# Kernel tuning notes

Hardware: AMD Instinct MI355X
Metric: run time of the kernel (lower is better)

The kernel has to match this reference:

```python
import jax, jax.numpy as jnp
import numpy as np

N_E = 1024      # nconcepts (codebook size)
E_DIM = 64      # cdim (codebook vector dim)
BETA = 0.25
LEGACY = True


def setup_inputs() -> dict:
    key = jax.random.key(0)
    k1, k2, k3 = jax.random.split(key, 3)
    z_ = jax.random.normal(k1, (32, 256, 32, 32), jnp.float32)
    # 1x1 conv dis_modulator: 256 -> 64 channels (stored as [out, in])
    conv_w = jax.random.normal(k2, (64, 256), jnp.float32) / np.sqrt(256.0)
    conv_b = jnp.zeros((64,), jnp.float32)
    # embedding.weight.data.uniform_(-1/n_e, 1/n_e)
    emb = jax.random.uniform(k3, (N_E, E_DIM), jnp.float32, -1.0 / N_E, 1.0 / N_E)
    return {"z_": z_, "conv_w": conv_w, "conv_b": conv_b, "emb": emb}


def _forward(z_, conv_w, conv_b, emb):
    sg = jax.lax.stop_gradient
    # dis_modulator: 1x1 conv == per-pixel linear map  (B,Cin,H,W)->(B,Cout,H,W)
    z = jnp.einsum('bchw,oc->bohw', z_, conv_w) + conv_b[None, :, None, None]
    B = z.shape[0]
    # torch .view(-1, e_dim): row-major flatten of (B,C,H,W) into chunks of e_dim
    zf = z.reshape(-1, E_DIM)  # [B*C*H*W/e_dim, e_dim]

    # contrastive term: mean pairwise cosine similarity of codebook rows
    d1 = emb @ emb.T                                  # [n_e, n_e]
    norms = jnp.linalg.norm(emb, axis=1)              # [n_e]
    cosine = d1 / (norms[:, None] * norms[None, :])
    contrastive = jnp.mean(cosine)

    # squared L2 distances: ||z||^2 + ||e||^2 - 2 z.e
    d = (jnp.sum(zf * zf, axis=1, keepdims=True)
         + jnp.sum(emb * emb, axis=1)[None, :]
         - 2.0 * (zf @ emb.T))                        # [N, n_e]
    idx = jnp.argmin(d, axis=1)                       # [N]
    z_q = emb[idx].reshape(z.shape)

    if LEGACY:
        loss = jnp.mean((sg(z_q) - z) ** 2) + BETA * jnp.mean((z_q - sg(z)) ** 2)
    else:
        loss = BETA * jnp.mean((sg(z_q) - z) ** 2) + jnp.mean((z_q - sg(z)) ** 2)
    # hessian_penalty(G, z_, G_z=z): G is an affine 1x1 conv, so the central
    # second difference G(z+x) - 2G(z) + G(z-x) is identically zero -> penalty = 0.
    loss = loss + contrastive

    # straight-through estimator
    z_q_st = z + sg(z_q - z)

    # replicate source exactly: flat zeros(B*n_e) scattered at codebook indices
    sampled = jnp.zeros((B * N_E,), z.dtype).at[idx].set(1.0).reshape(B, N_E)
    min_idx = idx.reshape(B, -1)
    return z_q_st, loss, sampled, min_idx


def reference(z_, conv_w, conv_b, emb):
    z_q, loss, sampled, min_idx = _forward(z_, conv_w, conv_b, emb)
    return z_q, loss, sampled, min_idx
```

## Files before the change

kernel.cpp:

```cpp
#include <hip/hip_runtime.h>
#include <hip/hip_bf16.h>

#define BATCH   32
#define CIN     256
#define COUT    64
#define HW      1024
#define NE      1024
#define ED      64
#define NROW    32768
#define ZTOT    2097152

#define OFF_LOSS 2097152
#define OFF_SAMP 2097153
#define OFF_IDX  2129921

#define XSTR 68
#define ESTR 132

__global__ __launch_bounds__(256) void k_init(float* __restrict__ out_samp,
                                              const float* __restrict__ emb,
                                              float* __restrict__ enorm,
                                              float* __restrict__ invn) {
    int b = blockIdx.x;
    if (b < 128) {
        int i = b * 256 + threadIdx.x;
        out_samp[i] = 0.0f;
    } else {
        int j = (b - 128) * 256 + threadIdx.x;
        const float* e = emb + j * ED;
        float r8[8];
        #pragma unroll
        for (int s = 0; s < 8; s++) { float x = e[s]; r8[s] = x * x; }
        #pragma unroll
        for (int m = 1; m < 8; m++) {
            #pragma unroll
            for (int s = 0; s < 8; s++) { float x = e[8 * m + s]; r8[s] += x * x; }
        }
        float en = ((r8[0] + r8[1]) + (r8[2] + r8[3])) + ((r8[4] + r8[5]) + (r8[6] + r8[7]));
        enorm[j] = en;
        invn[j]  = 1.0f / sqrtf(en);
    }
}

__global__ __launch_bounds__(256) void k_contrast(const float* __restrict__ emb,
                                                  const float* __restrict__ invn,
                                                  float* __restrict__ cpart) {
    int t = threadIdx.x;
    int b = blockIdx.x;
    int d = t & 63, q = t >> 6;
    int i0 = b * 64;
    float s = 0.0f;
    #pragma unroll
    for (int m = 0; m < 16; m++) {
        int i = i0 + q + 4 * m;
        s = fmaf(emb[i * ED + d], invn[i], s);
    }
    __shared__ float S[256];
    S[t] = s;
    __syncthreads();
    if (t < 64)
        cpart[b * 64 + t] = (S[t] + S[t + 64]) + (S[t + 128] + S[t + 192]);
}

__global__ __launch_bounds__(256) void k_conv(const float* __restrict__ x,
                                              const float* __restrict__ w,
                                              const float* __restrict__ bias,
                                              float* __restrict__ z) {
    __shared__ float Xs[64 * XSTR];
    __shared__ float Ws[64 * XSTR];
    int t  = threadIdx.x;
    int b  = blockIdx.y;
    int p0 = blockIdx.x * 64;
    int pg = t & 15;
    int og = t >> 4;
    float acc[4][4];
    #pragma unroll
    for (int i = 0; i < 4; i++)
        #pragma unroll
        for (int j = 0; j < 4; j++) acc[i][j] = 0.0f;

    for (int c0 = 0; c0 < CIN; c0 += 64) {
        __syncthreads();
        {
            int u = t & 15, cg2 = t >> 4;
            #pragma unroll
            for (int m = 0; m < 4; m++) {
                int c = cg2 + 16 * m;
                float4 v = *(const float4*)&x[(size_t)(b * CIN + c0 + c) * HW + p0 + 4 * u];
                *(float4*)&Xs[c * XSTR + 4 * u] = v;
            }
            #pragma unroll
            for (int m = 0; m < 4; m++) {
                int o = cg2 + 16 * m;
                float4 v = *(const float4*)&w[o * CIN + c0 + 4 * u];
                Ws[(4 * u + 0) * XSTR + o] = v.x;
                Ws[(4 * u + 1) * XSTR + o] = v.y;
                Ws[(4 * u + 2) * XSTR + o] = v.z;
                Ws[(4 * u + 3) * XSTR + o] = v.w;
            }
        }
        __syncthreads();
        #pragma unroll 8
        for (int k = 0; k < 64; k++) {
            float4 xv = *(const float4*)&Xs[k * XSTR + 4 * pg];
            float4 wv = *(const float4*)&Ws[k * XSTR + 4 * og];
            float xa[4] = {xv.x, xv.y, xv.z, xv.w};
            float wb[4] = {wv.x, wv.y, wv.z, wv.w};
            #pragma unroll
            for (int i = 0; i < 4; i++)
                #pragma unroll
                for (int j = 0; j < 4; j++)
                    acc[i][j] = fmaf(xa[i], wb[j], acc[i][j]);
        }
    }
    #pragma unroll
    for (int j = 0; j < 4; j++) {
        int o = 4 * og + j;
        float bv = bias[o];
        float4 out;
        out.x = acc[0][j] + bv;
        out.y = acc[1][j] + bv;
        out.z = acc[2][j] + bv;
        out.w = acc[3][j] + bv;
        *(float4*)&z[(size_t)(b * COUT + o) * HW + p0 + 4 * pg] = out;
    }
}

__global__ __launch_bounds__(256) void k_dist(const float* __restrict__ z,
                                              const float* __restrict__ emb,
                                              const float* __restrict__ enorm,
                                              float* __restrict__ out_idx,
                                              float* __restrict__ out_samp,
                                              float* __restrict__ out_zq,
                                              float* __restrict__ ssep) {
    __shared__ float zs[64 * XSTR];
    __shared__ float es[64 * ESTR];
    __shared__ float zn_s[64];
    __shared__ float en_s[128];
    __shared__ float redd_s[16 * 64];
    __shared__ int   redj_s[16 * 64];
    __shared__ int   bj_s[64];
    __shared__ float warr[4];
    int t = threadIdx.x;
    int row0 = blockIdx.x * 64;
    int rg = t & 15;
    int cg = t >> 4;

    {
        int k = t & 63, wv = t >> 6;
        #pragma unroll
        for (int m = 0; m < 4; m++) {
            int v = wv + 4 * m;
            float4 val;
            val.x = z[(size_t)(row0 + 4 * v + 0) * ED + k];
            val.y = z[(size_t)(row0 + 4 * v + 1) * ED + k];
            val.z = z[(size_t)(row0 + 4 * v + 2) * ED + k];
            val.w = z[(size_t)(row0 + 4 * v + 3) * ED + k];
            *(float4*)&zs[k * XSTR + 4 * v] = val;
        }
    }
    if (t < 64) {
        const float* zr = z + (size_t)(row0 + t) * ED;
        float r8[8];
        #pragma unroll
        for (int s = 0; s < 8; s++) { float xx = zr[s]; r8[s] = xx * xx; }
        #pragma unroll
        for (int m = 1; m < 8; m++) {
            #pragma unroll
            for (int s = 0; s < 8; s++) { float xx = zr[8 * m + s]; r8[s] += xx * xx; }
        }
        zn_s[t] = ((r8[0] + r8[1]) + (r8[2] + r8[3])) + ((r8[4] + r8[5]) + (r8[6] + r8[7]));
    }

    float bestd[4];
    int   bestj[4];
    #pragma unroll
    for (int i = 0; i < 4; i++) { bestd[i] = __builtin_huge_valf(); bestj[i] = 0; }

    for (int ch = 0; ch < 8; ch++) {
        int c0 = ch * 128;
        __syncthreads();
        {
            int k = t & 63, wv = t >> 6;
            #pragma unroll
            for (int m = 0; m < 8; m++) {
                int v = wv + 4 * m;
                float4 val;
                val.x = emb[(size_t)(c0 + 4 * v + 0) * ED + k];
                val.y = emb[(size_t)(c0 + 4 * v + 1) * ED + k];
                val.z = emb[(size_t)(c0 + 4 * v + 2) * ED + k];
                val.w = emb[(size_t)(c0 + 4 * v + 3) * ED + k];
                *(float4*)&es[k * ESTR + 4 * v] = val;
            }
            if (t < 32) {
                float4 ev4 = *(const float4*)&enorm[c0 + 4 * t];
                *(float4*)&en_s[4 * t] = ev4;
            }
        }
        __syncthreads();

        float acc[4][8];
        #pragma unroll
        for (int i = 0; i < 4; i++)
            #pragma unroll
            for (int j = 0; j < 8; j++) acc[i][j] = 0.0f;

        #pragma unroll 8
        for (int k = 0; k < 64; k++) {
            float4 xv = *(const float4*)&zs[k * XSTR + 4 * rg];
            float4 e0 = *(const float4*)&es[k * ESTR + 8 * cg];
            float4 e1 = *(const float4*)&es[k * ESTR + 8 * cg + 4];
            float xa[4] = {xv.x, xv.y, xv.z, xv.w};
            float eb[8] = {e0.x, e0.y, e0.z, e0.w, e1.x, e1.y, e1.z, e1.w};
            #pragma unroll
            for (int i = 0; i < 4; i++)
                #pragma unroll
                for (int j = 0; j < 8; j++)
                    acc[i][j] = fmaf(xa[i], eb[j], acc[i][j]);
        }

        #pragma unroll
        for (int i = 0; i < 4; i++) {
            float zn = zn_s[4 * rg + i];
            #pragma unroll
            for (int j = 0; j < 8; j++) {
                int cl = 8 * cg + j;
                float A = zn + en_s[cl];
                float D = A - 2.0f * acc[i][j];
                if (D < bestd[i]) { bestd[i] = D; bestj[i] = c0 + cl; }
            }
        }
    }

    #pragma unroll
    for (int i = 0; i < 4; i++) {
        redd_s[cg * 64 + 4 * rg + i] = bestd[i];
        redj_s[cg * 64 + 4 * rg + i] = bestj[i];
    }
    __syncthreads();
    if (t < 64) {
        float bd = __builtin_huge_valf();
        int   bj = 0x7fffffff;
        #pragma unroll
        for (int c = 0; c < 16; c++) {
            float dd = redd_s[c * 64 + t];
            int   jj = redj_s[c * 64 + t];
            if (dd < bd || (dd == bd && jj < bj)) { bd = dd; bj = jj; }
        }
        int rowg = row0 + t;
        bj_s[t]       = bj;
        out_idx[rowg] = (float)bj;
        atomicExch(&out_samp[bj], 1.0f);
    }
    __syncthreads();

    {
        int r  = t & 63;
        int kq = t >> 6;
        int bj = bj_s[r];
        const float* er = emb + (size_t)bj * ED + kq * 16;
        float sq = 0.0f;
        #pragma unroll
        for (int m = 0; m < 4; m++) {
            float4 ev = *(const float4*)&er[4 * m];
            float zv0 = zs[(kq * 16 + 4 * m + 0) * XSTR + r];
            float zv1 = zs[(kq * 16 + 4 * m + 1) * XSTR + r];
            float zv2 = zs[(kq * 16 + 4 * m + 2) * XSTR + r];
            float zv3 = zs[(kq * 16 + 4 * m + 3) * XSTR + r];
            float d0 = ev.x - zv0, d1 = ev.y - zv1, d2 = ev.z - zv2, d3 = ev.w - zv3;
            float4 o4;
            o4.x = zv0 + d0; o4.y = zv1 + d1; o4.z = zv2 + d2; o4.w = zv3 + d3;
            *(float4*)&out_zq[(size_t)(row0 + r) * ED + kq * 16 + 4 * m] = o4;
            sq += d0 * d0; sq += d1 * d1; sq += d2 * d2; sq += d3 * d3;
        }
        #pragma unroll
        for (int off = 32; off > 0; off >>= 1) sq += __shfl_down(sq, off, 64);
        int lane = t & 63, wv = t >> 6;
        if (lane == 0) warr[wv] = sq;
    }
    __syncthreads();
    if (t == 0)
        ssep[blockIdx.x] = (warr[0] + warr[1]) + (warr[2] + warr[3]);
}

__global__ __launch_bounds__(256) void k_final(const float* __restrict__ ssep,
                                               const float* __restrict__ cpart,
                                               float* __restrict__ out_loss) {
    __shared__ double SD[256];
    __shared__ float  CS;
    int t = threadIdx.x;
    SD[t] = (double)ssep[t] + (double)ssep[t + 256];
    __syncthreads();
    #pragma unroll
    for (int off = 128; off > 0; off >>= 1) {
        if (t < off) SD[t] += SD[t + off];
        __syncthreads();
    }
    if (t < 64) {
        float v = 0.0f;
        #pragma unroll
        for (int m = 0; m < 16; m++) v += cpart[m * 64 + t];
        float sq = v * v;
        #pragma unroll
        for (int off = 32; off > 0; off >>= 1) sq += __shfl_down(sq, off, 64);
        if (t == 0) CS = sq / (1024.0f * 1024.0f);
    }
    __syncthreads();
    if (t == 0) {
        float m = (float)(SD[0] / (double)ZTOT);
        float loss = m + 0.25f * m;
        out_loss[0] = loss + CS;
    }
}

extern "C" void kernel_launch(void* const* d_in, const int* in_sizes, int n_in,
                              void* d_out, int out_size, void* d_ws, size_t ws_size,
                              hipStream_t stream) {
    (void)in_sizes; (void)n_in; (void)out_size; (void)ws_size;
    const float* z_     = (const float*)d_in[0];
    const float* conv_w = (const float*)d_in[1];
    const float* conv_b = (const float*)d_in[2];
    const float* emb    = (const float*)d_in[3];

    float* out      = (float*)d_out;
    float* out_zq   = out;
    float* out_loss = out + OFF_LOSS;
    float* out_samp = out + OFF_SAMP;
    float* out_idx  = out + OFF_IDX;

    char*  ws       = (char*)d_ws;
    float* wz       = (float*)ws;
    float* enorm    = (float*)(ws + 8388608);
    float* invn     = enorm + 1024;
    float* cpart    = (float*)(ws + 8396800);
    float* ssep     = (float*)(ws + 8400896);

    k_init    <<<132, 256, 0, stream>>>(out_samp, emb, enorm, invn);
    k_contrast<<<16,  256, 0, stream>>>(emb, invn, cpart);
    k_conv    <<<dim3(16, 32), 256, 0, stream>>>(z_, conv_w, conv_b, wz);
    k_dist    <<<512, 256, 0, stream>>>(wz, emb, enorm, out_idx, out_samp, out_zq, ssep);
    k_final   <<<1, 256, 0, stream>>>(ssep, cpart, out_loss);
}
```

Baseline: 166.3 us.

## Merge init/contrast/conv into one launch and enlarge conv and distance tiles

Folds the sampled-buffer zeroing, codebook norms, contrastive partial sums and the 1x1 conv into a single k_pre launch that branches on block index, dropping two kernel launches. Conv tiles grow to 128 pixels per block (8x4 per thread) and the distance kernel handles 128 rows by 256 codes per chunk with an 8x16 per-thread accumulator, which raises register reuse but leaves only 256 blocks at one block per CU. The z-norm now reads from shared memory, and the reduction buffers reuse the codebook tile storage. The larger accumulators may push up register pressure and lower occupancy.

```diff
diff --git a/kernel.cpp b/kernel.cpp
--- a/kernel.cpp
+++ b/kernel.cpp
@@ -1,5 +1,4 @@
 #include <hip/hip_runtime.h>
-#include <hip/hip_bf16.h>
 
 #define BATCH   32
 #define CIN     256
@@ -14,100 +13,118 @@
 #define OFF_SAMP 2097153
 #define OFF_IDX  2129921
 
-#define XSTR 68
-#define ESTR 132
-
-__global__ __launch_bounds__(256) void k_init(float* __restrict__ out_samp,
-                                              const float* __restrict__ emb,
-                                              float* __restrict__ enorm,
-                                              float* __restrict__ invn) {
-    int b = blockIdx.x;
-    if (b < 128) {
-        int i = b * 256 + threadIdx.x;
-        out_samp[i] = 0.0f;
-    } else {
-        int j = (b - 128) * 256 + threadIdx.x;
-        const float* e = emb + j * ED;
+#define CXSTR 132
+#define CWSTR 68
+#define ZSTR  132
+#define ESTR2 260
+
+__global__ __launch_bounds__(256, 2) void k_pre(const float* __restrict__ x,
+                                                const float* __restrict__ w,
+                                                const float* __restrict__ bias,
+                                                float* __restrict__ z,
+                                                const float* __restrict__ emb,
+                                                float* __restrict__ out_samp,
+                                                float* __restrict__ enorm,
+                                                float* __restrict__ cpart) {
+    __shared__ float SH[64 * CXSTR + 64 * CWSTR];
+    int bx = blockIdx.x;
+    int t  = threadIdx.x;
+
+    if (bx < 128) {
+        out_samp[bx * 256 + t] = 0.0f;
+        return;
+    }
+    if (bx < 144) {
+        float* invl = SH;
+        float* S    = SH + 64;
+        int b2 = bx - 128;
+        int i0 = b2 * 64;
+        if (t < 64) {
+            const float* e = emb + (size_t)(i0 + t) * ED;
+            float r8[8];
+            #pragma unroll
+            for (int s = 0; s < 8; s++) { float xx = e[s]; r8[s] = xx * xx; }
+            #pragma unroll
+            for (int m = 1; m < 8; m++) {
+                #pragma unroll
+                for (int s = 0; s < 8; s++) { float xx = e[8 * m + s]; r8[s] += xx * xx; }
+            }
+            float en = ((r8[0] + r8[1]) + (r8[2] + r8[3])) + ((r8[4] + r8[5]) + (r8[6] + r8[7]));
+            invl[t] = 1.0f / sqrtf(en);
+        }
+        __syncthreads();
+        int d = t & 63, q = t >> 6;
+        float s = 0.0f;
+        #pragma unroll
+        for (int m = 0; m < 16; m++) {
+            int il = q + 4 * m;
+            s = fmaf(emb[(size_t)(i0 + il) * ED + d], invl[il], s);
+        }
+        S[t] = s;
+        __syncthreads();
+        if (t < 64)
+            cpart[b2 * 64 + t] = (S[t] + S[t + 64]) + (S[t + 128] + S[t + 192]);
+        return;
+    }
+    if (bx < 148) {
+        int j = (bx - 144) * 256 + t;
+        const float* e = emb + (size_t)j * ED;
         float r8[8];
         #pragma unroll
-        for (int s = 0; s < 8; s++) { float x = e[s]; r8[s] = x * x; }
+        for (int s = 0; s < 8; s++) { float xx = e[s]; r8[s] = xx * xx; }
         #pragma unroll
         for (int m = 1; m < 8; m++) {
             #pragma unroll
-            for (int s = 0; s < 8; s++) { float x = e[8 * m + s]; r8[s] += x * x; }
-        }
-        float en = ((r8[0] + r8[1]) + (r8[2] + r8[3])) + ((r8[4] + r8[5]) + (r8[6] + r8[7]));
-        enorm[j] = en;
-        invn[j]  = 1.0f / sqrtf(en);
-    }
-}
-
-__global__ __launch_bounds__(256) void k_contrast(const float* __restrict__ emb,
-                                                  const float* __restrict__ invn,
-                                                  float* __restrict__ cpart) {
-    int t = threadIdx.x;
-    int b = blockIdx.x;
-    int d = t & 63, q = t >> 6;
-    int i0 = b * 64;
-    float s = 0.0f;
-    #pragma unroll
-    for (int m = 0; m < 16; m++) {
-        int i = i0 + q + 4 * m;
-        s = fmaf(emb[i * ED + d], invn[i], s);
-    }
-    __shared__ float S[256];
-    S[t] = s;
-    __syncthreads();
-    if (t < 64)
-        cpart[b * 64 + t] = (S[t] + S[t + 64]) + (S[t + 128] + S[t + 192]);
-}
-
-__global__ __launch_bounds__(256) void k_conv(const float* __restrict__ x,
-                                              const float* __restrict__ w,
-                                              const float* __restrict__ bias,
-                                              float* __restrict__ z) {
-    __shared__ float Xs[64 * XSTR];
-    __shared__ float Ws[64 * XSTR];
-    int t  = threadIdx.x;
-    int b  = blockIdx.y;
-    int p0 = blockIdx.x * 64;
-    int pg = t & 15;
-    int og = t >> 4;
-    float acc[4][4];
-    #pragma unroll
-    for (int i = 0; i < 4; i++)
+            for (int s = 0; s < 8; s++) { float xx = e[8 * m + s]; r8[s] += xx * xx; }
+        }
+        enorm[j] = ((r8[0] + r8[1]) + (r8[2] + r8[3])) + ((r8[4] + r8[5]) + (r8[6] + r8[7]));
+        return;
+    }
+
+    float* Xs = SH;
+    float* Ws = SH + 64 * CXSTR;
+    int cbx = bx - 148;
+    int b   = cbx >> 3;
+    int p0  = (cbx & 7) * 128;
+    int pg  = t & 15;
+    int og  = t >> 4;
+    float acc[8][4];
+    #pragma unroll
+    for (int i = 0; i < 8; i++)
         #pragma unroll
         for (int j = 0; j < 4; j++) acc[i][j] = 0.0f;
 
     for (int c0 = 0; c0 < CIN; c0 += 64) {
         __syncthreads();
         {
-            int u = t & 15, cg2 = t >> 4;
+            int u = t & 31, cc = t >> 5;
+            #pragma unroll
+            for (int m = 0; m < 8; m++) {
+                int c = cc + 8 * m;
+                float4 v = *(const float4*)&x[(size_t)(b * CIN + c0 + c) * HW + p0 + 4 * u];
+                *(float4*)&Xs[c * CXSTR + 4 * u] = v;
+            }
+            int u2 = t & 15, o2 = t >> 4;
             #pragma unroll
             for (int m = 0; m < 4; m++) {
-                int c = cg2 + 16 * m;
-                float4 v = *(const float4*)&x[(size_t)(b * CIN + c0 + c) * HW + p0 + 4 * u];
-                *(float4*)&Xs[c * XSTR + 4 * u] = v;
-            }
-            #pragma unroll
-            for (int m = 0; m < 4; m++) {
-                int o = cg2 + 16 * m;
-                float4 v = *(const float4*)&w[o * CIN + c0 + 4 * u];
-                Ws[(4 * u + 0) * XSTR + o] = v.x;
-                Ws[(4 * u + 1) * XSTR + o] = v.y;
-                Ws[(4 * u + 2) * XSTR + o] = v.z;
-                Ws[(4 * u + 3) * XSTR + o] = v.w;
-            }
-        }
-        __syncthreads();
-        #pragma unroll 8
+                int o = o2 + 16 * m;
+                float4 v = *(const float4*)&w[o * CIN + c0 + 4 * u2];
+                Ws[(4 * u2 + 0) * CWSTR + o] = v.x;
+                Ws[(4 * u2 + 1) * CWSTR + o] = v.y;
+                Ws[(4 * u2 + 2) * CWSTR + o] = v.z;
+                Ws[(4 * u2 + 3) * CWSTR + o] = v.w;
+            }
+        }
+        __syncthreads();
+        #pragma unroll 4
         for (int k = 0; k < 64; k++) {
-            float4 xv = *(const float4*)&Xs[k * XSTR + 4 * pg];
-            float4 wv = *(const float4*)&Ws[k * XSTR + 4 * og];
-            float xa[4] = {xv.x, xv.y, xv.z, xv.w};
-            float wb[4] = {wv.x, wv.y, wv.z, wv.w};
-            #pragma unroll
-            for (int i = 0; i < 4; i++)
+            float4 xa4 = *(const float4*)&Xs[k * CXSTR + 4 * pg];
+            float4 xb4 = *(const float4*)&Xs[k * CXSTR + 64 + 4 * pg];
+            float4 wv4 = *(const float4*)&Ws[k * CWSTR + 4 * og];
+            float xa[8] = {xa4.x, xa4.y, xa4.z, xa4.w, xb4.x, xb4.y, xb4.z, xb4.w};
+            float wb[4] = {wv4.x, wv4.y, wv4.z, wv4.w};
+            #pragma unroll
+            for (int i = 0; i < 8; i++)
                 #pragma unroll
                 for (int j = 0; j < 4; j++)
                     acc[i][j] = fmaf(xa[i], wb[j], acc[i][j]);
@@ -117,114 +134,120 @@
     for (int j = 0; j < 4; j++) {
         int o = 4 * og + j;
         float bv = bias[o];
-        float4 out;
-        out.x = acc[0][j] + bv;
-        out.y = acc[1][j] + bv;
-        out.z = acc[2][j] + bv;
-        out.w = acc[3][j] + bv;
-        *(float4*)&z[(size_t)(b * COUT + o) * HW + p0 + 4 * pg] = out;
+        float4 lo, hi;
+        lo.x = acc[0][j] + bv; lo.y = acc[1][j] + bv;
+        lo.z = acc[2][j] + bv; lo.w = acc[3][j] + bv;
+        hi.x = acc[4][j] + bv; hi.y = acc[5][j] + bv;
+        hi.z = acc[6][j] + bv; hi.w = acc[7][j] + bv;
+        *(float4*)&z[(size_t)(b * COUT + o) * HW + p0 + 4 * pg]      = lo;
+        *(float4*)&z[(size_t)(b * COUT + o) * HW + p0 + 64 + 4 * pg] = hi;
     }
 }
 
-__global__ __launch_bounds__(256) void k_dist(const float* __restrict__ z,
-                                              const float* __restrict__ emb,
-                                              const float* __restrict__ enorm,
-                                              float* __restrict__ out_idx,
-                                              float* __restrict__ out_samp,
-                                              float* __restrict__ out_zq,
-                                              float* __restrict__ ssep) {
-    __shared__ float zs[64 * XSTR];
-    __shared__ float es[64 * ESTR];
-    __shared__ float zn_s[64];
-    __shared__ float en_s[128];
-    __shared__ float redd_s[16 * 64];
-    __shared__ int   redj_s[16 * 64];
-    __shared__ int   bj_s[64];
+__global__ __launch_bounds__(256, 1) void k_dist(const float* __restrict__ z,
+                                                 const float* __restrict__ emb,
+                                                 const float* __restrict__ enorm,
+                                                 float* __restrict__ out_idx,
+                                                 float* __restrict__ out_samp,
+                                                 float* __restrict__ out_zq,
+                                                 float* __restrict__ ssep) {
+    __shared__ float zs[64 * ZSTR];
+    __shared__ float es[64 * ESTR2];
+    __shared__ float zn_s[128];
+    __shared__ float en_s[256];
     __shared__ float warr[4];
+    float* redd_s = es;
+    int*   redj_s = (int*)(es + 2048);
+    int*   bj_s   = (int*)(es + 4096);
     int t = threadIdx.x;
-    int row0 = blockIdx.x * 64;
+    int row0 = blockIdx.x * 128;
     int rg = t & 15;
     int cg = t >> 4;
 
     {
         int k = t & 63, wv = t >> 6;
         #pragma unroll
-        for (int m = 0; m < 4; m++) {
+        for (int m = 0; m < 8; m++) {
             int v = wv + 4 * m;
             float4 val;
             val.x = z[(size_t)(row0 + 4 * v + 0) * ED + k];
             val.y = z[(size_t)(row0 + 4 * v + 1) * ED + k];
             val.z = z[(size_t)(row0 + 4 * v + 2) * ED + k];
             val.w = z[(size_t)(row0 + 4 * v + 3) * ED + k];
-            *(float4*)&zs[k * XSTR + 4 * v] = val;
-        }
-    }
-    if (t < 64) {
-        const float* zr = z + (size_t)(row0 + t) * ED;
+            *(float4*)&zs[k * ZSTR + 4 * v] = val;
+        }
+    }
+    __syncthreads();
+    if (t < 128) {
         float r8[8];
         #pragma unroll
-        for (int s = 0; s < 8; s++) { float xx = zr[s]; r8[s] = xx * xx; }
+        for (int s = 0; s < 8; s++) { float xx = zs[s * ZSTR + t]; r8[s] = xx * xx; }
         #pragma unroll
         for (int m = 1; m < 8; m++) {
             #pragma unroll
-            for (int s = 0; s < 8; s++) { float xx = zr[8 * m + s]; r8[s] += xx * xx; }
+            for (int s = 0; s < 8; s++) { float xx = zs[(8 * m + s) * ZSTR + t]; r8[s] += xx * xx; }
         }
         zn_s[t] = ((r8[0] + r8[1]) + (r8[2] + r8[3])) + ((r8[4] + r8[5]) + (r8[6] + r8[7]));
     }
 
-    float bestd[4];
-    int   bestj[4];
-    #pragma unroll
-    for (int i = 0; i < 4; i++) { bestd[i] = __builtin_huge_valf(); bestj[i] = 0; }
-
-    for (int ch = 0; ch < 8; ch++) {
-        int c0 = ch * 128;
+    float bestd[8];
+    int   bestj[8];
+    #pragma unroll
+    for (int i = 0; i < 8; i++) { bestd[i] = __builtin_huge_valf(); bestj[i] = 0; }
+
+    for (int ch = 0; ch < 4; ch++) {
+        int c0 = ch * 256;
         __syncthreads();
         {
             int k = t & 63, wv = t >> 6;
             #pragma unroll
-            for (int m = 0; m < 8; m++) {
+            for (int m = 0; m < 16; m++) {
                 int v = wv + 4 * m;
                 float4 val;
                 val.x = emb[(size_t)(c0 + 4 * v + 0) * ED + k];
                 val.y = emb[(size_t)(c0 + 4 * v + 1) * ED + k];
                 val.z = emb[(size_t)(c0 + 4 * v + 2) * ED + k];
                 val.w = emb[(size_t)(c0 + 4 * v + 3) * ED + k];
-                *(float4*)&es[k * ESTR + 4 * v] = val;
-            }
-            if (t < 32) {
+                *(float4*)&es[k * ESTR2 + 4 * v] = val;
+            }
+            if (t < 64) {
                 float4 ev4 = *(const float4*)&enorm[c0 + 4 * t];
                 *(float4*)&en_s[4 * t] = ev4;
             }
         }
         __syncthreads();
 
-        float acc[4][8];
-        #pragma unroll
-        for (int i = 0; i < 4; i++)
-            #pragma unroll
-            for (int j = 0; j < 8; j++) acc[i][j] = 0.0f;
-
-        #pragma unroll 8
+        float acc[8][16];
+        #pragma unroll
+        for (int i = 0; i < 8; i++)
+            #pragma unroll
+            for (int j = 0; j < 16; j++) acc[i][j] = 0.0f;
+
+        #pragma unroll 2
         for (int k = 0; k < 64; k++) {
-            float4 xv = *(const float4*)&zs[k * XSTR + 4 * rg];
-            float4 e0 = *(const float4*)&es[k * ESTR + 8 * cg];
-            float4 e1 = *(const float4*)&es[k * ESTR + 8 * cg + 4];
-            float xa[4] = {xv.x, xv.y, xv.z, xv.w};
-            float eb[8] = {e0.x, e0.y, e0.z, e0.w, e1.x, e1.y, e1.z, e1.w};
-            #pragma unroll
-            for (int i = 0; i < 4; i++)
+            float4 za = *(const float4*)&zs[k * ZSTR + 4 * rg];
+            float4 zb = *(const float4*)&zs[k * ZSTR + 64 + 4 * rg];
+            float4 e0 = *(const float4*)&es[k * ESTR2 + 16 * cg];
+            float4 e1 = *(const float4*)&es[k * ESTR2 + 16 * cg + 4];
+            float4 e2 = *(const float4*)&es[k * ESTR2 + 16 * cg + 8];
+            float4 e3 = *(const float4*)&es[k * ESTR2 + 16 * cg + 12];
+            float xa[8]  = {za.x, za.y, za.z, za.w, zb.x, zb.y, zb.z, zb.w};
+            float eb[16] = {e0.x, e0.y, e0.z, e0.w, e1.x, e1.y, e1.z, e1.w,
+                            e2.x, e2.y, e2.z, e2.w, e3.x, e3.y, e3.z, e3.w};
+            #pragma unroll
+            for (int i = 0; i < 8; i++)
                 #pragma unroll
-                for (int j = 0; j < 8; j++)
+                for (int j = 0; j < 16; j++)
                     acc[i][j] = fmaf(xa[i], eb[j], acc[i][j]);
         }
 
         #pragma unroll
-        for (int i = 0; i < 4; i++) {
-            float zn = zn_s[4 * rg + i];
-            #pragma unroll
-            for (int j = 0; j < 8; j++) {
-                int cl = 8 * cg + j;
+        for (int i = 0; i < 8; i++) {
+            int rl = (i < 4) ? (4 * rg + i) : (64 + 4 * rg + (i - 4));
+            float zn = zn_s[rl];
+            #pragma unroll
+            for (int j = 0; j < 16; j++) {
+                int cl = 16 * cg + j;
                 float A = zn + en_s[cl];
                 float D = A - 2.0f * acc[i][j];
                 if (D < bestd[i]) { bestd[i] = D; bestj[i] = c0 + cl; }
@@ -232,19 +255,21 @@
         }
     }
 
-    #pragma unroll
-    for (int i = 0; i < 4; i++) {
-        redd_s[cg * 64 + 4 * rg + i] = bestd[i];
-        redj_s[cg * 64 + 4 * rg + i] = bestj[i];
-    }
-    __syncthreads();
-    if (t < 64) {
+    __syncthreads();
+    #pragma unroll
+    for (int i = 0; i < 8; i++) {
+        int rl = (i < 4) ? (4 * rg + i) : (64 + 4 * rg + (i - 4));
+        redd_s[cg * 128 + rl] = bestd[i];
+        redj_s[cg * 128 + rl] = bestj[i];
+    }
+    __syncthreads();
+    if (t < 128) {
         float bd = __builtin_huge_valf();
         int   bj = 0x7fffffff;
         #pragma unroll
         for (int c = 0; c < 16; c++) {
-            float dd = redd_s[c * 64 + t];
-            int   jj = redj_s[c * 64 + t];
+            float dd = redd_s[c * 128 + t];
+            int   jj = redj_s[c * 128 + t];
             if (dd < bd || (dd == bd && jj < bj)) { bd = dd; bj = jj; }
         }
         int rowg = row0 + t;
@@ -255,28 +280,28 @@
     __syncthreads();
 
     {
-        int r  = t & 63;
-        int kq = t >> 6;
+        int r  = t & 127;
+        int kq = t >> 7;
         int bj = bj_s[r];
-        const float* er = emb + (size_t)bj * ED + kq * 16;
+        const float* er = emb + (size_t)bj * ED + kq * 32;
         float sq = 0.0f;
         #pragma unroll
-        for (int m = 0; m < 4; m++) {
+        for (int m = 0; m < 8; m++) {
             float4 ev = *(const float4*)&er[4 * m];
-            float zv0 = zs[(kq * 16 + 4 * m + 0) * XSTR + r];
-            float zv1 = zs[(kq * 16 + 4 * m + 1) * XSTR + r];
-            float zv2 = zs[(kq * 16 + 4 * m + 2) * XSTR + r];
-            float zv3 = zs[(kq * 16 + 4 * m + 3) * XSTR + r];
+            int kk = kq * 32 + 4 * m;
+            float zv0 = zs[(kk + 0) * ZSTR + r];
+            float zv1 = zs[(kk + 1) * ZSTR + r];
+            float zv2 = zs[(kk + 2) * ZSTR + r];
+            float zv3 = zs[(kk + 3) * ZSTR + r];
             float d0 = ev.x - zv0, d1 = ev.y - zv1, d2 = ev.z - zv2, d3 = ev.w - zv3;
             float4 o4;
             o4.x = zv0 + d0; o4.y = zv1 + d1; o4.z = zv2 + d2; o4.w = zv3 + d3;
-            *(float4*)&out_zq[(size_t)(row0 + r) * ED + kq * 16 + 4 * m] = o4;
+            *(float4*)&out_zq[(size_t)(row0 + r) * ED + kk] = o4;
             sq += d0 * d0; sq += d1 * d1; sq += d2 * d2; sq += d3 * d3;
         }
         #pragma unroll
         for (int off = 32; off > 0; off >>= 1) sq += __shfl_down(sq, off, 64);
-        int lane = t & 63, wv = t >> 6;
-        if (lane == 0) warr[wv] = sq;
+        if ((t & 63) == 0) warr[t >> 6] = sq;
     }
     __syncthreads();
     if (t == 0)
@@ -289,7 +314,7 @@
     __shared__ double SD[256];
     __shared__ float  CS;
     int t = threadIdx.x;
-    SD[t] = (double)ssep[t] + (double)ssep[t + 256];
+    SD[t] = (double)ssep[t];
     __syncthreads();
     #pragma unroll
     for (int off = 128; off > 0; off >>= 1) {
@@ -331,13 +356,10 @@
     char*  ws       = (char*)d_ws;
     float* wz       = (float*)ws;
     float* enorm    = (float*)(ws + 8388608);
-    float* invn     = enorm + 1024;
     float* cpart    = (float*)(ws + 8396800);
     float* ssep     = (float*)(ws + 8400896);
 
-    k_init    <<<132, 256, 0, stream>>>(out_samp, emb, enorm, invn);
-    k_contrast<<<16,  256, 0, stream>>>(emb, invn, cpart);
-    k_conv    <<<dim3(16, 32), 256, 0, stream>>>(z_, conv_w, conv_b, wz);
-    k_dist    <<<512, 256, 0, stream>>>(wz, emb, enorm, out_idx, out_samp, out_zq, ssep);
-    k_final   <<<1, 256, 0, stream>>>(ssep, cpart, out_loss);
+    k_pre  <<<404, 256, 0, stream>>>(z_, conv_w, conv_b, wz, emb, out_samp, enorm, cpart);
+    k_dist <<<256, 256, 0, stream>>>(wz, emb, enorm, out_idx, out_samp, out_zq, ssep);
+    k_final<<<1,   256, 0, stream>>>(ssep, cpart, out_loss);
 }
```

Result: slower. 179.5 us (+8.0%).
